# Kernel optimization log

Hardware: AMD Instinct MI355X
Metric: run time of the kernel (lower is better)

The kernel has to match this reference:

```python
import jax, jax.numpy as jnp
import numpy as np
from jax import lax

B, T_DEC, T_ENC = 32, 64, 256
H, E, V = 512, 512, 32000
L, NH = 2, 8
EPS = 1e-5


def setup_inputs() -> dict:
    key = jax.random.key(0)
    ks = jax.random.split(key, 18)
    n = jax.random.normal
    s = 0.02
    return {
        "x": jax.random.randint(ks[0], (B, T_DEC), 0, V),
        "enc_outputs": n(ks[1], (B, T_ENC, 2 * H)),
        "hidden_state": n(ks[2], (L, B, H)),
        "enc_valid_lens": jax.random.randint(ks[3], (B,), 1, T_ENC + 1),
        "emb": n(ks[4], (V, E)) * s,
        "W_q": n(ks[5], (H, H)) * s,
        "W_k": n(ks[6], (2 * H, H)) * s,
        "W_v": n(ks[7], (2 * H, H)) * s,
        "W_o": n(ks[8], (H, H)) * s,
        "W_in": n(ks[9], (E + H, H)) * s,
        "ln_gamma": jnp.ones((L, H)),
        "ln_beta": jnp.zeros((L, H)),
        "alphas": n(ks[10], (L,)) * 0.1,
        "W_ih": n(ks[11], (L, 3 * H, H)) * s,
        "W_hh": n(ks[12], (L, 3 * H, H)) * s,
        "b_ih": n(ks[13], (L, 3 * H)) * s,
        "b_hh": n(ks[14], (L, 3 * H)) * s,
        "W_dense": n(ks[15], (H, V)) * s,
        "b_dense": n(ks[16], (V,)) * s,
    }


def _layernorm(x, g, b):
    mu = jnp.mean(x, -1, keepdims=True)
    var = jnp.var(x, -1, keepdims=True)
    return (x - mu) * lax.rsqrt(var + EPS) * g + b


def _gru_cell(x, h, Wih, Whh, bih, bhh):
    # PyTorch GRU cell math
    gi = x @ Wih.T + bih
    gh = h @ Whh.T + bhh
    ir, iz, ig = jnp.split(gi, 3, -1)
    hr, hz, hg = jnp.split(gh, 3, -1)
    r = jax.nn.sigmoid(ir + hr)
    z = jax.nn.sigmoid(iz + hz)
    g = jnp.tanh(ig + r * hg)
    return (1.0 - z) * g + z * h


def _decode(x, enc_outputs, hidden_state, enc_valid_lens, emb, W_q, W_k, W_v, W_o,
            W_in, ln_gamma, ln_beta, alphas, W_ih, W_hh, b_ih, b_hh, W_dense, b_dense):
    dh = H // NH
    scale = 1.0 / np.sqrt(dh).astype(np.float32)
    # keys/values depend only on enc_outputs -> hoist out of decode loop
    Kh = (enc_outputs @ W_k).reshape(B, T_ENC, NH, dh)
    Vh = (enc_outputs @ W_v).reshape(B, T_ENC, NH, dh)
    key_mask = jnp.arange(T_ENC)[None, :] < enc_valid_lens[:, None]  # [B,S]
    emb_seq = jnp.transpose(emb[x], (1, 0, 2))  # [T,B,E]

    def step(h, e_t):
        # single-query multi-head attention against encoder outputs
        q = (h[-1] @ W_q).reshape(B, NH, dh)
        scores = jnp.einsum('bhd,bshd->bhs', q, Kh) * scale
        scores = jnp.where(key_mask[:, None, :], scores, -1e6)
        attn = jax.nn.softmax(scores, axis=-1)
        ctx = jnp.einsum('bhs,bshd->bhd', attn, Vh).reshape(B, H) @ W_o
        # ResNormGRU: in_proj, then per-layer LN -> GRU step -> alpha residual
        xr = jnp.concatenate([ctx, e_t], -1) @ W_in  # [B,H]
        hs = []
        for i in range(L):
            xin = _layernorm(xr, ln_gamma[i], ln_beta[i])
            hi = _gru_cell(xin, h[i], W_ih[i], W_hh[i], b_ih[i], b_hh[i])
            xr = xr + alphas[i] * hi  # GRU output y == new hidden for T=1
            hs.append(hi)
        return jnp.stack(hs), xr

    hN, ys = lax.scan(step, hidden_state, emb_seq)  # ys: [T,B,H]
    logits = ys @ W_dense + b_dense  # [T,B,V]
    return jnp.transpose(logits, (1, 0, 2)), hN


def reference(x, enc_outputs, hidden_state, enc_valid_lens, emb, W_q, W_k, W_v, W_o,
              W_in, ln_gamma, ln_beta, alphas, W_ih, W_hh, b_ih, b_hh, W_dense, b_dense):
    return _decode(x, enc_outputs, hidden_state, enc_valid_lens, emb, W_q, W_k, W_v, W_o,
                   W_in, ln_gamma, ln_beta, alphas, W_ih, W_hh, b_ih, b_hh, W_dense, b_dense)
```

## Files before the change

### kernel.cpp

```cpp
#include <hip/hip_runtime.h>
#include <math.h>

#define TDEC 64
#define TENC 256
#define BB   32
#define HH   512
#define VV   32000

typedef short bf16x8 __attribute__((ext_vector_type(8)));
typedef float f32x4  __attribute__((ext_vector_type(4)));

__device__ __forceinline__ float bf2f(short u) {
  union { unsigned int i; float f; } c;
  c.i = ((unsigned int)(unsigned short)u) << 16;
  return c.f;
}
__device__ __forceinline__ short f2bf(float f) {
  union { float f; unsigned int i; } c; c.f = f;
  unsigned int x = c.i;
  unsigned int r = (x + 0x7fffu + ((x >> 16) & 1u)) >> 16;
  return (short)r;
}

template <int AMODE, int SMODE>
__global__ __launch_bounds__(256) void gemm_k(
    const void* __restrict__ Ap, const short* __restrict__ BT,
    void* __restrict__ Cp, int M, int N, int K,
    const int* __restrict__ gidx, const float* __restrict__ gsrc,
    const float* __restrict__ bias)
{
  __shared__ short As[128 * 72];
  __shared__ short Bs[128 * 72];
  const int tid = threadIdx.x;
  const int n0 = blockIdx.x * 128, m0 = blockIdx.y * 128;
  const int w = tid >> 6, lane = tid & 63;
  const int wm = (w >> 1) * 64, wn = (w & 1) * 64;

  f32x4 acc[4][4] = {};

  for (int k0 = 0; k0 < K; k0 += 64) {
    #pragma unroll
    for (int i = 0; i < 4; ++i) {
      int cc = i * 256 + tid;
      int row = cc >> 3, col = (cc & 7) * 8;
      if constexpr (AMODE == 0) {
        const short* A = (const short*)Ap;
        *(bf16x8*)&As[row * 72 + col] =
            *(const bf16x8*)&A[(size_t)(m0 + row) * K + k0 + col];
      } else {
        const float* src;
        if constexpr (AMODE == 1) {
          src = (const float*)Ap + (size_t)(m0 + row) * K + k0 + col;
        } else {
          int r = m0 + row, tt = r >> 5, bb = r & 31;
          src = gsrc + (size_t)gidx[bb * 64 + tt] * 512 + k0 + col;
        }
        float4 f0 = *(const float4*)&src[0];
        float4 f1 = *(const float4*)&src[4];
        short tmp[8] = { f2bf(f0.x), f2bf(f0.y), f2bf(f0.z), f2bf(f0.w),
                         f2bf(f1.x), f2bf(f1.y), f2bf(f1.z), f2bf(f1.w) };
        *(bf16x8*)&As[row * 72 + col] = *(bf16x8*)tmp;
      }
      *(bf16x8*)&Bs[row * 72 + col] =
          *(const bf16x8*)&BT[(size_t)(n0 + row) * K + k0 + col];
    }
    __syncthreads();

    #pragma unroll
    for (int kk = 0; kk < 2; ++kk) {
      const int kcol = kk * 32 + (lane >> 4) * 8;
      bf16x8 af[4], bfr[4];
      #pragma unroll
      for (int mi = 0; mi < 4; ++mi)
        af[mi] = *(const bf16x8*)&As[(wm + mi * 16 + (lane & 15)) * 72 + kcol];
      #pragma unroll
      for (int ni = 0; ni < 4; ++ni)
        bfr[ni] = *(const bf16x8*)&Bs[(wn + ni * 16 + (lane & 15)) * 72 + kcol];
      #pragma unroll
      for (int mi = 0; mi < 4; ++mi)
        #pragma unroll
        for (int ni = 0; ni < 4; ++ni)
          acc[mi][ni] = __builtin_amdgcn_mfma_f32_16x16x32_bf16(
              af[mi], bfr[ni], acc[mi][ni], 0, 0, 0);
    }
    __syncthreads();
  }

  #pragma unroll
  for (int mi = 0; mi < 4; ++mi) {
    #pragma unroll
    for (int ni = 0; ni < 4; ++ni) {
      int col = n0 + wn + ni * 16 + (lane & 15);
      #pragma unroll
      for (int r = 0; r < 4; ++r) {
        int row = m0 + wm + mi * 16 + ((lane >> 4) * 4) + r;
        float v = acc[mi][ni][r];
        if constexpr (SMODE == 0) {
          ((float*)Cp)[(size_t)row * N + col] = v;
        } else if constexpr (SMODE == 1) {
          int b = row >> 8, s = row & 255, h = col >> 6, d = col & 63;
          ((short*)Cp)[(size_t)((b * 8 + h) * 256 + s) * 64 + d] = f2bf(v);
        } else {
          int tt = row >> 5, b = row & 31;
          ((float*)Cp)[(size_t)(b * 64 + tt) * N + col] = v + bias[col];
        }
      }
    }
  }
}

template <typename OT>
__global__ __launch_bounds__(256) void transpose_k(
    const float* __restrict__ in, OT* __restrict__ out, int Rin, int Cin)
{
  __shared__ float tile[32][33];
  int c0 = blockIdx.x * 32, r0 = blockIdx.y * 32;
  int ci = threadIdx.x & 31, rg = threadIdx.x >> 5;
  #pragma unroll
  for (int i = 0; i < 4; ++i) {
    int r = rg * 4 + i;
    tile[r][ci] = in[(size_t)(r0 + r) * Cin + c0 + ci];
  }
  __syncthreads();
  #pragma unroll
  for (int i = 0; i < 4; ++i) {
    int rr = rg * 4 + i;
    float v = tile[ci][rr];
    if constexpr (sizeof(OT) == 2)
      out[(size_t)(c0 + rr) * Rin + r0 + ci] = f2bf(v);
    else
      out[(size_t)(c0 + rr) * Rin + r0 + ci] = v;
  }
}

__global__ void init_k(const float* __restrict__ hs,
                       float* __restrict__ h0, float* __restrict__ h1)
{
  int i = blockIdx.x * 256 + threadIdx.x;
  h0[i] = hs[i];
  h1[i] = hs[16384 + i];
}

__global__ void fin_k(const float* __restrict__ h0, const float* __restrict__ h1,
                      float* __restrict__ out2)
{
  int i = blockIdx.x * 256 + threadIdx.x;
  out2[i] = h0[i];
  out2[16384 + i] = h1[i];
}

__global__ __launch_bounds__(512) void attnxr_k(
    const float* __restrict__ h1, const float* __restrict__ Wq,
    const short* __restrict__ Kbf, const short* __restrict__ Vbf,
    const int* __restrict__ vlen, const float* __restrict__ Wcmb,
    const float* __restrict__ Eproj_t, float* __restrict__ xr)
{
  __shared__ float hq[512];
  __shared__ float ql[512];
  __shared__ float attn[8 * 256];
  __shared__ float rc[512];
  const int b = blockIdx.x;
  const int tid = threadIdx.x;

  hq[tid] = h1[b * 512 + tid];
  __syncthreads();

  {
    float a = 0.f;
    #pragma unroll 8
    for (int e = 0; e < 512; ++e) a += hq[e] * Wq[e * 512 + tid];
    ql[tid] = a;
  }
  __syncthreads();

  const int h = tid >> 6, lane = tid & 63;
  const int L = vlen[b];
  {
    const short* Kb = Kbf + (size_t)((b * 8 + h) * 256) * 64;
    const float* qh = &ql[h * 64];
    float sc[4];
    #pragma unroll
    for (int i = 0; i < 4; ++i) {
      int s = lane + i * 64;
      const short* kr = Kb + s * 64;
      float a = 0.f;
      #pragma unroll
      for (int d0 = 0; d0 < 64; d0 += 8) {
        bf16x8 kv = *(const bf16x8*)&kr[d0];
        #pragma unroll
        for (int e = 0; e < 8; ++e) a += qh[d0 + e] * bf2f(kv[e]);
      }
      sc[i] = (s < L) ? a * 0.125f : -1e30f;
    }
    float m = fmaxf(fmaxf(sc[0], sc[1]), fmaxf(sc[2], sc[3]));
    #pragma unroll
    for (int off = 32; off > 0; off >>= 1) m = fmaxf(m, __shfl_xor(m, off, 64));
    float ex[4], sum = 0.f;
    #pragma unroll
    for (int i = 0; i < 4; ++i) {
      ex[i] = (sc[i] > -1e29f) ? __expf(sc[i] - m) : 0.f;
      sum += ex[i];
    }
    #pragma unroll
    for (int off = 32; off > 0; off >>= 1) sum += __shfl_xor(sum, off, 64);
    float inv = 1.f / sum;
    #pragma unroll
    for (int i = 0; i < 4; ++i) attn[h * 256 + lane + i * 64] = ex[i] * inv;
  }
  __syncthreads();

  {
    const short* Vb = Vbf + (size_t)((b * 8 + h) * 256) * 64;
    const float* at = &attn[h * 256];
    float a = 0.f;
    #pragma unroll 4
    for (int s = 0; s < 256; ++s) a += at[s] * bf2f(Vb[s * 64 + lane]);
    rc[tid] = a;
  }
  __syncthreads();

  {
    float a = 0.f;
    #pragma unroll 8
    for (int e = 0; e < 512; ++e) a += rc[e] * Wcmb[e * 512 + tid];
    xr[b * 512 + tid] = a + Eproj_t[b * 512 + tid];
  }
}

__global__ __launch_bounds__(512) void gru_k(
    const float* __restrict__ xr_in, float* __restrict__ xr_out,
    const float* __restrict__ h_in, float* __restrict__ h_out,
    const float* __restrict__ Wih, const float* __restrict__ Whh,
    const float* __restrict__ bih, const float* __restrict__ bhh,
    const float* __restrict__ gamma, const float* __restrict__ beta,
    const float* __restrict__ alphas, int layer, short* __restrict__ ys_t)
{
  __shared__ float xl[32 * 513];
  __shared__ float hl[32 * 513];
  __shared__ float ps[32 * 16];
  __shared__ float pq[32 * 16];
  __shared__ float mu[32];
  __shared__ float rsd[32];
  __shared__ float red[6 * 512];
  const int tid = threadIdx.x;

  {
    int b = tid >> 4, seg = tid & 15;
    const float* xs = xr_in + b * 512 + seg * 32;
    const float* hs = h_in + b * 512 + seg * 32;
    float* xd = xl + b * 513 + seg * 32;
    float* hd = hl + b * 513 + seg * 32;
    float s = 0.f, q = 0.f;
    #pragma unroll
    for (int i = 0; i < 32; i += 4) {
      float4 v = *(const float4*)(xs + i);
      xd[i] = v.x; xd[i + 1] = v.y; xd[i + 2] = v.z; xd[i + 3] = v.w;
      s += v.x + v.y + v.z + v.w;
      q += v.x * v.x + v.y * v.y + v.z * v.z + v.w * v.w;
      float4 u = *(const float4*)(hs + i);
      hd[i] = u.x; hd[i + 1] = u.y; hd[i + 2] = u.z; hd[i + 3] = u.w;
    }
    ps[tid] = s; pq[tid] = q;
  }
  __syncthreads();
  if (tid < 32) {
    float s = 0.f, q = 0.f;
    #pragma unroll
    for (int i = 0; i < 16; ++i) { s += ps[tid * 16 + i]; q += pq[tid * 16 + i]; }
    float m = s * (1.f / 512.f);
    mu[tid] = m;
    rsd[tid] = rsqrtf(q * (1.f / 512.f) - m * m + 1e-5f);
  }
  __syncthreads();
  {
    int b = tid >> 4, seg = tid & 15;
    float m = mu[b], r = rsd[b];
    float* xd = xl + b * 513 + seg * 32;
    const float* g = gamma + seg * 32;
    const float* be = beta + seg * 32;
    #pragma unroll
    for (int i = 0; i < 32; ++i) xd[i] = (xd[i] - m) * r * g[i] + be[i];
  }
  __syncthreads();

  const int b = tid & 31, qe = (tid >> 5) & 3, jj = tid >> 7;
  const int j = blockIdx.x * 4 + jj;
  const float* xb = xl + b * 513;
  const float* hb = hl + b * 513;
  const float* wiR = Wih + (size_t)j * 512;
  const float* wiZ = Wih + (size_t)(512 + j) * 512;
  const float* wiG = Wih + (size_t)(1024 + j) * 512;
  const float* whR = Whh + (size_t)j * 512;
  const float* whZ = Whh + (size_t)(512 + j) * 512;
  const float* whG = Whh + (size_t)(1024 + j) * 512;
  float aR = 0.f, aZ = 0.f, aG = 0.f, cR = 0.f, cZ = 0.f, cG = 0.f;
  const int e0 = qe * 128;
  for (int e = e0; e < e0 + 128; e += 4) {
    float4 w1 = *(const float4*)(wiR + e);
    float4 w2 = *(const float4*)(wiZ + e);
    float4 w3 = *(const float4*)(wiG + e);
    float4 u1 = *(const float4*)(whR + e);
    float4 u2 = *(const float4*)(whZ + e);
    float4 u3 = *(const float4*)(whG + e);
    float x0 = xb[e], x1 = xb[e + 1], x2 = xb[e + 2], x3 = xb[e + 3];
    float y0 = hb[e], y1 = hb[e + 1], y2 = hb[e + 2], y3 = hb[e + 3];
    aR += x0 * w1.x + x1 * w1.y + x2 * w1.z + x3 * w1.w;
    aZ += x0 * w2.x + x1 * w2.y + x2 * w2.z + x3 * w2.w;
    aG += x0 * w3.x + x1 * w3.y + x2 * w3.z + x3 * w3.w;
    cR += y0 * u1.x + y1 * u1.y + y2 * u1.z + y3 * u1.w;
    cZ += y0 * u2.x + y1 * u2.y + y2 * u2.z + y3 * u2.w;
    cG += y0 * u3.x + y1 * u3.y + y2 * u3.z + y3 * u3.w;
  }
  red[tid] = aR;         red[512 + tid] = aZ;  red[1024 + tid] = aG;
  red[1536 + tid] = cR;  red[2048 + tid] = cZ; red[2560 + tid] = cG;
  __syncthreads();

  if (qe == 0) {
    int base = jj * 128 + b;
    float giR = red[base] + red[base + 32] + red[base + 64] + red[base + 96] + bih[j];
    float giZ = red[512 + base] + red[512 + base + 32] + red[512 + base + 64] + red[512 + base + 96] + bih[512 + j];
    float giG = red[1024 + base] + red[1024 + base + 32] + red[1024 + base + 64] + red[1024 + base + 96] + bih[1024 + j];
    float ghR = red[1536 + base] + red[1536 + base + 32] + red[1536 + base + 64] + red[1536 + base + 96] + bhh[j];
    float ghZ = red[2048 + base] + red[2048 + base + 32] + red[2048 + base + 64] + red[2048 + base + 96] + bhh[512 + j];
    float ghG = red[2560 + base] + red[2560 + base + 32] + red[2560 + base + 64] + red[2560 + base + 96] + bhh[1024 + j];
    float r = 1.f / (1.f + __expf(-(giR + ghR)));
    float z = 1.f / (1.f + __expf(-(giZ + ghZ)));
    float g = tanhf(giG + r * ghG);
    float hp = hb[j];
    float hn = (1.f - z) * g + z * hp;
    h_out[b * 512 + j] = hn;
    float xv = xr_in[b * 512 + j] + alphas[layer] * hn;
    xr_out[b * 512 + j] = xv;
    if (ys_t) ys_t[b * 512 + j] = f2bf(xv);
  }
}

extern "C" void kernel_launch(void* const* d_in, const int* in_sizes, int n_in,
                              void* d_out, int out_size, void* d_ws, size_t ws_size,
                              hipStream_t stream)
{
  (void)in_sizes; (void)n_in; (void)out_size; (void)ws_size;
  const int*   x     = (const int*)d_in[0];
  const float* enc   = (const float*)d_in[1];
  const float* hs    = (const float*)d_in[2];
  const int*   vlen  = (const int*)d_in[3];
  const float* emb   = (const float*)d_in[4];
  const float* Wq    = (const float*)d_in[5];
  const float* Wk    = (const float*)d_in[6];
  const float* Wv    = (const float*)d_in[7];
  const float* Wo    = (const float*)d_in[8];
  const float* Win   = (const float*)d_in[9];
  const float* lng   = (const float*)d_in[10];
  const float* lnb   = (const float*)d_in[11];
  const float* alph  = (const float*)d_in[12];
  const float* Wih   = (const float*)d_in[13];
  const float* Whh   = (const float*)d_in[14];
  const float* bih   = (const float*)d_in[15];
  const float* bhh   = (const float*)d_in[16];
  const float* Wd    = (const float*)d_in[17];
  const float* bd    = (const float*)d_in[18];
  float* out = (float*)d_out;

  char* ws = (char*)d_ws;
  size_t off = 0;
  auto alloc = [&](size_t bytes) -> void* {
    void* p = ws + off;
    off = (off + bytes + 255) & ~(size_t)255;
    return p;
  };
  short* Kbf     = (short*)alloc((size_t)32 * 8 * 256 * 64 * 2);
  short* Vbf     = (short*)alloc((size_t)32 * 8 * 256 * 64 * 2);
  short* WkT     = (short*)alloc((size_t)512 * 1024 * 2);
  short* WvT     = (short*)alloc((size_t)512 * 1024 * 2);
  short* WdT     = (short*)alloc((size_t)32000 * 512 * 2);
  short* WinTopT = (short*)alloc((size_t)512 * 512 * 2);
  short* WinBotT = (short*)alloc((size_t)512 * 512 * 2);
  float* Wcmb    = (float*)alloc((size_t)512 * 512 * 4);
  float* Eproj   = (float*)alloc((size_t)2048 * 512 * 4);
  float* xr0     = (float*)alloc((size_t)32 * 512 * 4);
  float* xr1     = (float*)alloc((size_t)32 * 512 * 4);
  float* h0a     = (float*)alloc((size_t)32 * 512 * 4);
  float* h0b     = (float*)alloc((size_t)32 * 512 * 4);
  float* h1a     = (float*)alloc((size_t)32 * 512 * 4);
  float* h1b     = (float*)alloc((size_t)32 * 512 * 4);
  short* ysbf    = (short*)alloc((size_t)2048 * 512 * 2);

  init_k<<<64, 256, 0, stream>>>(hs, h0a, h1a);

  transpose_k<short><<<dim3(16, 32), 256, 0, stream>>>(Wk, WkT, 1024, 512);
  transpose_k<short><<<dim3(16, 32), 256, 0, stream>>>(Wv, WvT, 1024, 512);
  transpose_k<short><<<dim3(1000, 16), 256, 0, stream>>>(Wd, WdT, 512, 32000);
  transpose_k<short><<<dim3(16, 16), 256, 0, stream>>>(Win, WinTopT, 512, 512);
  transpose_k<short><<<dim3(16, 16), 256, 0, stream>>>(Win + 512 * 512, WinBotT, 512, 512);

  gemm_k<1, 1><<<dim3(4, 64), 256, 0, stream>>>(enc, WkT, Kbf, 8192, 512, 1024, nullptr, nullptr, nullptr);
  gemm_k<1, 1><<<dim3(4, 64), 256, 0, stream>>>(enc, WvT, Vbf, 8192, 512, 1024, nullptr, nullptr, nullptr);
  gemm_k<1, 0><<<dim3(4, 4), 256, 0, stream>>>(Wo, WinTopT, Wcmb, 512, 512, 512, nullptr, nullptr, nullptr);
  gemm_k<2, 0><<<dim3(4, 16), 256, 0, stream>>>(nullptr, WinBotT, Eproj, 2048, 512, 512, x, emb, nullptr);

  for (int t = 0; t < 64; ++t) {
    const float* h0i = (t & 1) ? h0b : h0a;  float* h0o = (t & 1) ? h0a : h0b;
    const float* h1i = (t & 1) ? h1b : h1a;  float* h1o = (t & 1) ? h1a : h1b;
    attnxr_k<<<32, 512, 0, stream>>>(h1i, Wq, Kbf, Vbf, vlen, Wcmb,
                                     Eproj + (size_t)t * 32 * 512, xr0);
    gru_k<<<128, 512, 0, stream>>>(xr0, xr1, h0i, h0o,
                                   Wih, Whh, bih, bhh, lng, lnb,
                                   alph, 0, nullptr);
    gru_k<<<128, 512, 0, stream>>>(xr1, xr0, h1i, h1o,
                                   Wih + (size_t)1536 * 512, Whh + (size_t)1536 * 512,
                                   bih + 1536, bhh + 1536, lng + 512, lnb + 512,
                                   alph, 1, ysbf + (size_t)t * 32 * 512);
  }

  gemm_k<0, 2><<<dim3(250, 16), 256, 0, stream>>>(ysbf, WdT, out, 2048, 32000, 512,
                                                  nullptr, nullptr, bd);
  fin_k<<<64, 256, 0, stream>>>(h0a, h1a, out + (size_t)65536000);
}
```

Measured before the change: 8.921 ms.

## Fuse decode loop into one persistent kernel with grid-wide barriers

Replaces the 192 per-step kernel launches (attention plus two GRU layers per timestep) with a single persistent kernel of 128 blocks. The blocks step through all 64 timesteps and synchronise between phases with a software grid barrier built on atomics. The aim is to remove per-launch overhead and the gaps between dependent launches. The cost is spin-wait barrier latency, and the design assumes all 128 blocks are co-resident, which holds on a 256-CU part.

```diff
diff --git a/kernel.cpp b/kernel.cpp
--- a/kernel.cpp
+++ b/kernel.cpp
@@ -6,6 +6,7 @@
 #define BB   32
 #define HH   512
 #define VV   32000
+#define NBLK 128
 
 typedef short bf16x8 __attribute__((ext_vector_type(8)));
 typedef float f32x4  __attribute__((ext_vector_type(4)));
@@ -134,11 +135,13 @@
 }
 
 __global__ void init_k(const float* __restrict__ hs,
-                       float* __restrict__ h0, float* __restrict__ h1)
+                       float* __restrict__ h0, float* __restrict__ h1,
+                       unsigned* __restrict__ bar)
 {
   int i = blockIdx.x * 256 + threadIdx.x;
   h0[i] = hs[i];
   h1[i] = hs[16384 + i];
+  if (blockIdx.x == 0 && threadIdx.x < 128) bar[threadIdx.x] = 0u;
 }
 
 __global__ void fin_k(const float* __restrict__ h0, const float* __restrict__ h1,
@@ -149,27 +152,43 @@
   out2[16384 + i] = h1[i];
 }
 
-__global__ __launch_bounds__(512) void attnxr_k(
+struct SmA { float hq[512]; float ql[512]; float attn[8 * 256]; float rc[512]; };
+struct SmG { float xl[32 * 513]; float hl[32 * 513]; float ps[512]; float pq[512];
+             float mu[32]; float rsd[32]; float red[6 * 512]; };
+union SmU { SmA a; SmG g; };
+
+__device__ __forceinline__ void gbar(unsigned* cnt, unsigned* epoch, unsigned target) {
+  __syncthreads();
+  if (threadIdx.x == 0) {
+    __threadfence();
+    unsigned prev = atomicAdd(cnt, 1u);
+    if (prev == (unsigned)(NBLK - 1)) {
+      atomicExch(cnt, 0u);
+      __threadfence();
+      atomicAdd(epoch, 1u);
+    } else {
+      while (atomicAdd(epoch, 0u) < target) __builtin_amdgcn_s_sleep(2);
+    }
+    __threadfence();
+  }
+  __syncthreads();
+}
+
+__device__ __forceinline__ void attn_phase(
+    SmA& s, int b, int tid,
     const float* __restrict__ h1, const float* __restrict__ Wq,
     const short* __restrict__ Kbf, const short* __restrict__ Vbf,
     const int* __restrict__ vlen, const float* __restrict__ Wcmb,
     const float* __restrict__ Eproj_t, float* __restrict__ xr)
 {
-  __shared__ float hq[512];
-  __shared__ float ql[512];
-  __shared__ float attn[8 * 256];
-  __shared__ float rc[512];
-  const int b = blockIdx.x;
-  const int tid = threadIdx.x;
-
-  hq[tid] = h1[b * 512 + tid];
+  s.hq[tid] = h1[b * 512 + tid];
   __syncthreads();
 
   {
     float a = 0.f;
     #pragma unroll 8
-    for (int e = 0; e < 512; ++e) a += hq[e] * Wq[e * 512 + tid];
-    ql[tid] = a;
+    for (int e = 0; e < 512; ++e) a += s.hq[e] * Wq[e * 512 + tid];
+    s.ql[tid] = a;
   }
   __syncthreads();
 
@@ -177,12 +196,12 @@
   const int L = vlen[b];
   {
     const short* Kb = Kbf + (size_t)((b * 8 + h) * 256) * 64;
-    const float* qh = &ql[h * 64];
+    const float* qh = &s.ql[h * 64];
     float sc[4];
     #pragma unroll
     for (int i = 0; i < 4; ++i) {
-      int s = lane + i * 64;
-      const short* kr = Kb + s * 64;
+      int ss = lane + i * 64;
+      const short* kr = Kb + ss * 64;
       float a = 0.f;
       #pragma unroll
       for (int d0 = 0; d0 < 64; d0 += 8) {
@@ -190,7 +209,7 @@
         #pragma unroll
         for (int e = 0; e < 8; ++e) a += qh[d0 + e] * bf2f(kv[e]);
       }
-      sc[i] = (s < L) ? a * 0.125f : -1e30f;
+      sc[i] = (ss < L) ? a * 0.125f : -1e30f;
     }
     float m = fmaxf(fmaxf(sc[0], sc[1]), fmaxf(sc[2], sc[3]));
     #pragma unroll
@@ -205,77 +224,69 @@
     for (int off = 32; off > 0; off >>= 1) sum += __shfl_xor(sum, off, 64);
     float inv = 1.f / sum;
     #pragma unroll
-    for (int i = 0; i < 4; ++i) attn[h * 256 + lane + i * 64] = ex[i] * inv;
+    for (int i = 0; i < 4; ++i) s.attn[h * 256 + lane + i * 64] = ex[i] * inv;
   }
   __syncthreads();
 
   {
     const short* Vb = Vbf + (size_t)((b * 8 + h) * 256) * 64;
-    const float* at = &attn[h * 256];
+    const float* at = &s.attn[h * 256];
     float a = 0.f;
     #pragma unroll 4
-    for (int s = 0; s < 256; ++s) a += at[s] * bf2f(Vb[s * 64 + lane]);
-    rc[tid] = a;
+    for (int ss = 0; ss < 256; ++ss) a += at[ss] * bf2f(Vb[ss * 64 + lane]);
+    s.rc[tid] = a;
   }
   __syncthreads();
 
   {
     float a = 0.f;
     #pragma unroll 8
-    for (int e = 0; e < 512; ++e) a += rc[e] * Wcmb[e * 512 + tid];
+    for (int e = 0; e < 512; ++e) a += s.rc[e] * Wcmb[e * 512 + tid];
     xr[b * 512 + tid] = a + Eproj_t[b * 512 + tid];
   }
 }
 
-__global__ __launch_bounds__(512) void gru_k(
+__device__ __forceinline__ void gru_phase(
+    SmG& s, int blk, int tid,
     const float* __restrict__ xr_in, float* __restrict__ xr_out,
     const float* __restrict__ h_in, float* __restrict__ h_out,
     const float* __restrict__ Wih, const float* __restrict__ Whh,
     const float* __restrict__ bih, const float* __restrict__ bhh,
     const float* __restrict__ gamma, const float* __restrict__ beta,
-    const float* __restrict__ alphas, int layer, short* __restrict__ ys_t)
-{
-  __shared__ float xl[32 * 513];
-  __shared__ float hl[32 * 513];
-  __shared__ float ps[32 * 16];
-  __shared__ float pq[32 * 16];
-  __shared__ float mu[32];
-  __shared__ float rsd[32];
-  __shared__ float red[6 * 512];
-  const int tid = threadIdx.x;
-
+    float alpha, short* __restrict__ ys_t)
+{
   {
     int b = tid >> 4, seg = tid & 15;
     const float* xs = xr_in + b * 512 + seg * 32;
     const float* hs = h_in + b * 512 + seg * 32;
-    float* xd = xl + b * 513 + seg * 32;
-    float* hd = hl + b * 513 + seg * 32;
-    float s = 0.f, q = 0.f;
+    float* xd = s.xl + b * 513 + seg * 32;
+    float* hd = s.hl + b * 513 + seg * 32;
+    float sm = 0.f, q = 0.f;
     #pragma unroll
     for (int i = 0; i < 32; i += 4) {
       float4 v = *(const float4*)(xs + i);
       xd[i] = v.x; xd[i + 1] = v.y; xd[i + 2] = v.z; xd[i + 3] = v.w;
-      s += v.x + v.y + v.z + v.w;
+      sm += v.x + v.y + v.z + v.w;
       q += v.x * v.x + v.y * v.y + v.z * v.z + v.w * v.w;
       float4 u = *(const float4*)(hs + i);
       hd[i] = u.x; hd[i + 1] = u.y; hd[i + 2] = u.z; hd[i + 3] = u.w;
     }
-    ps[tid] = s; pq[tid] = q;
+    s.ps[tid] = sm; s.pq[tid] = q;
   }
   __syncthreads();
   if (tid < 32) {
-    float s = 0.f, q = 0.f;
-    #pragma unroll
-    for (int i = 0; i < 16; ++i) { s += ps[tid * 16 + i]; q += pq[tid * 16 + i]; }
-    float m = s * (1.f / 512.f);
-    mu[tid] = m;
-    rsd[tid] = rsqrtf(q * (1.f / 512.f) - m * m + 1e-5f);
+    float sm = 0.f, q = 0.f;
+    #pragma unroll
+    for (int i = 0; i < 16; ++i) { sm += s.ps[tid * 16 + i]; q += s.pq[tid * 16 + i]; }
+    float m = sm * (1.f / 512.f);
+    s.mu[tid] = m;
+    s.rsd[tid] = rsqrtf(q * (1.f / 512.f) - m * m + 1e-5f);
   }
   __syncthreads();
   {
     int b = tid >> 4, seg = tid & 15;
-    float m = mu[b], r = rsd[b];
-    float* xd = xl + b * 513 + seg * 32;
+    float m = s.mu[b], r = s.rsd[b];
+    float* xd = s.xl + b * 513 + seg * 32;
     const float* g = gamma + seg * 32;
     const float* be = beta + seg * 32;
     #pragma unroll
@@ -284,9 +295,9 @@
   __syncthreads();
 
   const int b = tid & 31, qe = (tid >> 5) & 3, jj = tid >> 7;
-  const int j = blockIdx.x * 4 + jj;
-  const float* xb = xl + b * 513;
-  const float* hb = hl + b * 513;
+  const int j = blk * 4 + jj;
+  const float* xb = s.xl + b * 513;
+  const float* hb = s.hl + b * 513;
   const float* wiR = Wih + (size_t)j * 512;
   const float* wiZ = Wih + (size_t)(512 + j) * 512;
   const float* wiG = Wih + (size_t)(1024 + j) * 512;
@@ -311,27 +322,74 @@
     cZ += y0 * u2.x + y1 * u2.y + y2 * u2.z + y3 * u2.w;
     cG += y0 * u3.x + y1 * u3.y + y2 * u3.z + y3 * u3.w;
   }
-  red[tid] = aR;         red[512 + tid] = aZ;  red[1024 + tid] = aG;
-  red[1536 + tid] = cR;  red[2048 + tid] = cZ; red[2560 + tid] = cG;
+  s.red[tid] = aR;         s.red[512 + tid] = aZ;  s.red[1024 + tid] = aG;
+  s.red[1536 + tid] = cR;  s.red[2048 + tid] = cZ; s.red[2560 + tid] = cG;
   __syncthreads();
 
   if (qe == 0) {
     int base = jj * 128 + b;
-    float giR = red[base] + red[base + 32] + red[base + 64] + red[base + 96] + bih[j];
-    float giZ = red[512 + base] + red[512 + base + 32] + red[512 + base + 64] + red[512 + base + 96] + bih[512 + j];
-    float giG = red[1024 + base] + red[1024 + base + 32] + red[1024 + base + 64] + red[1024 + base + 96] + bih[1024 + j];
-    float ghR = red[1536 + base] + red[1536 + base + 32] + red[1536 + base + 64] + red[1536 + base + 96] + bhh[j];
-    float ghZ = red[2048 + base] + red[2048 + base + 32] + red[2048 + base + 64] + red[2048 + base + 96] + bhh[512 + j];
-    float ghG = red[2560 + base] + red[2560 + base + 32] + red[2560 + base + 64] + red[2560 + base + 96] + bhh[1024 + j];
+    float giR = s.red[base] + s.red[base + 32] + s.red[base + 64] + s.red[base + 96] + bih[j];
+    float giZ = s.red[512 + base] + s.red[512 + base + 32] + s.red[512 + base + 64] + s.red[512 + base + 96] + bih[512 + j];
+    float giG = s.red[1024 + base] + s.red[1024 + base + 32] + s.red[1024 + base + 64] + s.red[1024 + base + 96] + bih[1024 + j];
+    float ghR = s.red[1536 + base] + s.red[1536 + base + 32] + s.red[1536 + base + 64] + s.red[1536 + base + 96] + bhh[j];
+    float ghZ = s.red[2048 + base] + s.red[2048 + base + 32] + s.red[2048 + base + 64] + s.red[2048 + base + 96] + bhh[512 + j];
+    float ghG = s.red[2560 + base] + s.red[2560 + base + 32] + s.red[2560 + base + 64] + s.red[2560 + base + 96] + bhh[1024 + j];
     float r = 1.f / (1.f + __expf(-(giR + ghR)));
     float z = 1.f / (1.f + __expf(-(giZ + ghZ)));
     float g = tanhf(giG + r * ghG);
     float hp = hb[j];
     float hn = (1.f - z) * g + z * hp;
     h_out[b * 512 + j] = hn;
-    float xv = xr_in[b * 512 + j] + alphas[layer] * hn;
+    float xv = xr_in[b * 512 + j] + alpha * hn;
     xr_out[b * 512 + j] = xv;
     if (ys_t) ys_t[b * 512 + j] = f2bf(xv);
+  }
+  __syncthreads();
+}
+
+__global__ __launch_bounds__(512) void scan_k(
+    const float* __restrict__ Wq,
+    const short* __restrict__ Kbf, const short* __restrict__ Vbf,
+    const int* __restrict__ vlen, const float* __restrict__ Wcmb,
+    const float* __restrict__ Eproj,
+    float* __restrict__ xr0, float* __restrict__ xr1,
+    float* __restrict__ h0a, float* __restrict__ h0b,
+    float* __restrict__ h1a, float* __restrict__ h1b,
+    const float* __restrict__ Wih, const float* __restrict__ Whh,
+    const float* __restrict__ bih, const float* __restrict__ bhh,
+    const float* __restrict__ lng, const float* __restrict__ lnb,
+    const float* __restrict__ alphas,
+    short* __restrict__ ysbf, unsigned* __restrict__ bar)
+{
+  __shared__ SmU sm;
+  const int blk = blockIdx.x, tid = threadIdx.x;
+  unsigned* cnt = bar;
+  unsigned* epoch = bar + 64;
+  unsigned ep = 0;
+
+  const float alpha0 = alphas[0], alpha1 = alphas[1];
+  float* h0i = h0a; float* h0o = h0b;
+  float* h1i = h1a; float* h1o = h1b;
+
+  for (int t = 0; t < 64; ++t) {
+    if (blk < 32)
+      attn_phase(sm.a, blk, tid, h1i, Wq, Kbf, Vbf, vlen, Wcmb,
+                 Eproj + (size_t)t * 32 * 512, xr0);
+    gbar(cnt, epoch, ++ep);
+
+    gru_phase(sm.g, blk, tid, xr0, xr1, h0i, h0o,
+              Wih, Whh, bih, bhh, lng, lnb, alpha0, nullptr);
+    gbar(cnt, epoch, ++ep);
+
+    gru_phase(sm.g, blk, tid, xr1, xr0, h1i, h1o,
+              Wih + (size_t)1536 * 512, Whh + (size_t)1536 * 512,
+              bih + 1536, bhh + 1536, lng + 512, lnb + 512,
+              alpha1, ysbf + (size_t)t * 32 * 512);
+    gbar(cnt, epoch, ++ep);
+
+    float* tp;
+    tp = h0i; h0i = h0o; h0o = tp;
+    tp = h1i; h1i = h1o; h1o = tp;
   }
 }
 
@@ -384,8 +442,9 @@
   float* h1a     = (float*)alloc((size_t)32 * 512 * 4);
   float* h1b     = (float*)alloc((size_t)32 * 512 * 4);
   short* ysbf    = (short*)alloc((size_t)2048 * 512 * 2);
-
-  init_k<<<64, 256, 0, stream>>>(hs, h0a, h1a);
+  unsigned* bar  = (unsigned*)alloc(512);
+
+  init_k<<<64, 256, 0, stream>>>(hs, h0a, h1a, bar);
 
   transpose_k<short><<<dim3(16, 32), 256, 0, stream>>>(Wk, WkT, 1024, 512);
   transpose_k<short><<<dim3(16, 32), 256, 0, stream>>>(Wv, WvT, 1024, 512);
@@ -398,19 +457,10 @@
   gemm_k<1, 0><<<dim3(4, 4), 256, 0, stream>>>(Wo, WinTopT, Wcmb, 512, 512, 512, nullptr, nullptr, nullptr);
   gemm_k<2, 0><<<dim3(4, 16), 256, 0, stream>>>(nullptr, WinBotT, Eproj, 2048, 512, 512, x, emb, nullptr);
 
-  for (int t = 0; t < 64; ++t) {
-    const float* h0i = (t & 1) ? h0b : h0a;  float* h0o = (t & 1) ? h0a : h0b;
-    const float* h1i = (t & 1) ? h1b : h1a;  float* h1o = (t & 1) ? h1a : h1b;
-    attnxr_k<<<32, 512, 0, stream>>>(h1i, Wq, Kbf, Vbf, vlen, Wcmb,
-                                     Eproj + (size_t)t * 32 * 512, xr0);
-    gru_k<<<128, 512, 0, stream>>>(xr0, xr1, h0i, h0o,
-                                   Wih, Whh, bih, bhh, lng, lnb,
-                                   alph, 0, nullptr);
-    gru_k<<<128, 512, 0, stream>>>(xr1, xr0, h1i, h1o,
-                                   Wih + (size_t)1536 * 512, Whh + (size_t)1536 * 512,
-                                   bih + 1536, bhh + 1536, lng + 512, lnb + 512,
-                                   alph, 1, ysbf + (size_t)t * 32 * 512);
-  }
+  scan_k<<<NBLK, 512, 0, stream>>>(Wq, Kbf, Vbf, vlen, Wcmb, Eproj,
+                                   xr0, xr1, h0a, h0b, h1a, h1b,
+                                   Wih, Whh, bih, bhh, lng, lnb, alph,
+                                   ysbf, bar);
 
   gemm_k<0, 2><<<dim3(250, 16), 256, 0, stream>>>(ysbf, WdT, out, 2048, 32000, 512,
                                                   nullptr, nullptr, bd);
```

Result: slower. 22.72 ms (+154.7%).
